# Performance work log

Measured on AMD Instinct MI355X. Metric: run time of the kernel, lower is better.

The kernel has to match this reference:

```python
import jax, jax.numpy as jnp
import numpy as np


def pairwise_distances(x):
    # x: [N, D] -> squared euclidean distances [N, N], clamped at 0
    sq = jnp.sum(x * x, axis=1)  # [N]
    dist = sq[:, None] + sq[None, :] - 2.0 * (x @ x.T)
    return jnp.maximum(dist, 0.0)


def setup_inputs() -> dict:
    key = jax.random.key(0)
    k1, k2 = jax.random.split(key)
    N, D, T = 8192, 128, 200000
    x = jax.random.normal(k1, (N, D), dtype=jnp.float32)
    triplets = jax.random.randint(k2, (T, 3), 0, N, dtype=jnp.int64)
    return {"x": x, "triplets": triplets}


def reference(x, triplets):
    dist = pairwise_distances(x)  # [N, N]
    i, j, k = triplets[:, 0], triplets[:, 1], triplets[:, 2]
    d_ij = dist[i, j]  # [T] anchor-positive distances
    d_ik = dist[i, k]  # [T] anchor-negative distances
    # loss = mean over triplets of log(1 + exp(d_ij - d_ik)) (uniform weights)
    loss = jnp.mean(jnp.log1p(jnp.exp(d_ij - d_ik)))
    return loss
```

## Files before the change

### kernel.cpp

```cpp
#include <hip/hip_runtime.h>
#include <math.h>

#define TRIP_BLOCKS 2048


template<int CTRL>
__device__ __forceinline__ float dpp_shr_add(float v) {
    int m = __builtin_amdgcn_update_dpp(0, __float_as_int(v), CTRL, 0xf, 0xf, true);
    return v + __int_as_float(m);
}

__device__ __forceinline__ float row16_sum(float v) {
    v = dpp_shr_add<0x111>(v);
    v = dpp_shr_add<0x112>(v);
    v = dpp_shr_add<0x114>(v);
    v = dpp_shr_add<0x118>(v);
    return v;
}

__device__ __forceinline__ float softplus_stable(float z) {
    return fmaxf(z, 0.0f) + log1pf(expf(-fabsf(z)));
}

__device__ __forceinline__ void sq_diff(const float4 a, const float4 b, float& acc) {
    float t;
    t = a.x - b.x; acc = fmaf(t, t, acc);
    t = a.y - b.y; acc = fmaf(t, t, acc);
    t = a.z - b.z; acc = fmaf(t, t, acc);
    t = a.w - b.w; acc = fmaf(t, t, acc);
}

__global__ void __launch_bounds__(256)
trip_kernel(const float* __restrict__ x, const int* __restrict__ trip,
            float* __restrict__ partial, int T) {
    const int lane    = threadIdx.x & 63;
    const int sub     = threadIdx.x & 15;
    const int gid     = (blockIdx.x * blockDim.x + threadIdx.x) >> 4;
    const int ngroups = (gridDim.x * blockDim.x) >> 4;

    const float4* xv = (const float4*)x;

    float local = 0.0f;
    for (int base = gid; base < T; base += 2 * ngroups) {
        int nA   = base;
        int nB   = base + ngroups;
        bool hasB = (nB < T);
        int nBc  = hasB ? nB : nA;

        int iA = trip[3 * nA], jA = trip[3 * nA + 1], kA = trip[3 * nA + 2];
        int iB = trip[3 * nBc], jB = trip[3 * nBc + 1], kB = trip[3 * nBc + 2];

        float4 aA0 = xv[iA * 32 + sub], aA1 = xv[iA * 32 + sub + 16];
        float4 bA0 = xv[jA * 32 + sub], bA1 = xv[jA * 32 + sub + 16];
        float4 cA0 = xv[kA * 32 + sub], cA1 = xv[kA * 32 + sub + 16];
        float4 aB0 = xv[iB * 32 + sub], aB1 = xv[iB * 32 + sub + 16];
        float4 bB0 = xv[jB * 32 + sub], bB1 = xv[jB * 32 + sub + 16];
        float4 cB0 = xv[kB * 32 + sub], cB1 = xv[kB * 32 + sub + 16];

        float d1A = 0.0f, d2A = 0.0f, d1B = 0.0f, d2B = 0.0f;
        sq_diff(aA0, bA0, d1A); sq_diff(aA1, bA1, d1A);
        sq_diff(aA0, cA0, d2A); sq_diff(aA1, cA1, d2A);
        sq_diff(aB0, bB0, d1B); sq_diff(aB1, bB1, d1B);
        sq_diff(aB0, cB0, d2B); sq_diff(aB1, cB1, d2B);

        d1A = row16_sum(d1A); d2A = row16_sum(d2A);
        d1B = row16_sum(d1B); d2B = row16_sum(d2B);

        if (sub == 15) {
            local += softplus_stable(d1A - d2A);
            if (hasB) local += softplus_stable(d1B - d2B);
        }
    }

    local += __shfl_xor(local, 16, 64);
    local += __shfl_xor(local, 32, 64);

    __shared__ float wsum[4];
    int wid = threadIdx.x >> 6;
    if (lane == 15) wsum[wid] = local;
    __syncthreads();
    if (threadIdx.x == 0)
        partial[blockIdx.x] = wsum[0] + wsum[1] + wsum[2] + wsum[3];
}

__global__ void __launch_bounds__(256)
finalize_kernel(const float* __restrict__ partial, int nparts,
                float* __restrict__ out, int T) {
    float s = 0.0f;
    for (int idx = threadIdx.x; idx < nparts; idx += 256)
        s += partial[idx];
#pragma unroll
    for (int off = 32; off; off >>= 1) s += __shfl_xor(s, off, 64);
    __shared__ float wsum[4];
    int wid = threadIdx.x >> 6;
    if ((threadIdx.x & 63) == 0) wsum[wid] = s;
    __syncthreads();
    if (threadIdx.x == 0)
        out[0] = (wsum[0] + wsum[1] + wsum[2] + wsum[3]) / (float)T;
}

extern "C" void kernel_launch(void* const* d_in, const int* in_sizes, int n_in,
                              void* d_out, int out_size, void* d_ws, size_t ws_size,
                              hipStream_t stream) {
    const float* x    = (const float*)d_in[0];
    const int*   trip = (const int*)d_in[1];
    float*       out  = (float*)d_out;

    int T = in_sizes[1] / 3;

    float* partial = (float*)d_ws;

    trip_kernel<<<TRIP_BLOCKS, 256, 0, stream>>>(x, trip, partial, T);
    finalize_kernel<<<1, 256, 0, stream>>>(partial, TRIP_BLOCKS, out, T);
}
```

Measured before the change: 78.20 us.

## Software-pipeline triplet index loads, drop dual-triplet unroll, use fast softplus

Replaces the two-triplets-per-iteration unroll with a single-triplet loop that prefetches the next triplet's indices while the current row gathers are in flight. The stable softplus switches to the fast __expf/__logf intrinsics, and the group count becomes a compile-time constant. The aim is to hide the dependent index-then-gather latency and cut transcendental cost. In exchange there are fewer independent gathers in flight per thread, slightly lower precision, and the code assumes the grid size always equals TRIP_BLOCKS.

```diff
diff --git a/kernel.cpp b/kernel.cpp
--- a/kernel.cpp
+++ b/kernel.cpp
@@ -18,8 +18,9 @@
     return v;
 }
 
-__device__ __forceinline__ float softplus_stable(float z) {
-    return fmaxf(z, 0.0f) + log1pf(expf(-fabsf(z)));
+__device__ __forceinline__ float softplus_fast(float z) {
+    float u = __expf(-fabsf(z));
+    return fmaxf(z, 0.0f) + __logf(1.0f + u);
 }
 
 __device__ __forceinline__ void sq_diff(const float4 a, const float4 b, float& acc) {
@@ -36,40 +37,41 @@
     const int lane    = threadIdx.x & 63;
     const int sub     = threadIdx.x & 15;
     const int gid     = (blockIdx.x * blockDim.x + threadIdx.x) >> 4;
-    const int ngroups = (gridDim.x * blockDim.x) >> 4;
+    const int ngroups = (TRIP_BLOCKS * 256) >> 4;
 
     const float4* xv = (const float4*)x;
 
     float local = 0.0f;
-    for (int base = gid; base < T; base += 2 * ngroups) {
-        int nA   = base;
-        int nB   = base + ngroups;
-        bool hasB = (nB < T);
-        int nBc  = hasB ? nB : nA;
 
-        int iA = trip[3 * nA], jA = trip[3 * nA + 1], kA = trip[3 * nA + 2];
-        int iB = trip[3 * nBc], jB = trip[3 * nBc + 1], kB = trip[3 * nBc + 2];
+    int n = gid;
+    int i = 0, j = 0, k = 0;
+    if (n < T) {
+        i = trip[3 * n];
+        j = trip[3 * n + 1];
+        k = trip[3 * n + 2];
+    }
+    while (n < T) {
+        float4 a0 = xv[i * 32 + sub], a1 = xv[i * 32 + sub + 16];
+        float4 b0 = xv[j * 32 + sub], b1 = xv[j * 32 + sub + 16];
+        float4 c0 = xv[k * 32 + sub], c1 = xv[k * 32 + sub + 16];
 
-        float4 aA0 = xv[iA * 32 + sub], aA1 = xv[iA * 32 + sub + 16];
-        float4 bA0 = xv[jA * 32 + sub], bA1 = xv[jA * 32 + sub + 16];
-        float4 cA0 = xv[kA * 32 + sub], cA1 = xv[kA * 32 + sub + 16];
-        float4 aB0 = xv[iB * 32 + sub], aB1 = xv[iB * 32 + sub + 16];
-        float4 bB0 = xv[jB * 32 + sub], bB1 = xv[jB * 32 + sub + 16];
-        float4 cB0 = xv[kB * 32 + sub], cB1 = xv[kB * 32 + sub + 16];
+        int n2 = n + ngroups;
+        if (n2 < T) {
+            i = trip[3 * n2];
+            j = trip[3 * n2 + 1];
+            k = trip[3 * n2 + 2];
+        }
 
-        float d1A = 0.0f, d2A = 0.0f, d1B = 0.0f, d2B = 0.0f;
-        sq_diff(aA0, bA0, d1A); sq_diff(aA1, bA1, d1A);
-        sq_diff(aA0, cA0, d2A); sq_diff(aA1, cA1, d2A);
-        sq_diff(aB0, bB0, d1B); sq_diff(aB1, bB1, d1B);
-        sq_diff(aB0, cB0, d2B); sq_diff(aB1, cB1, d2B);
+        float d1 = 0.0f, d2 = 0.0f;
+        sq_diff(a0, b0, d1); sq_diff(a1, b1, d1);
+        sq_diff(a0, c0, d2); sq_diff(a1, c1, d2);
 
-        d1A = row16_sum(d1A); d2A = row16_sum(d2A);
-        d1B = row16_sum(d1B); d2B = row16_sum(d2B);
+        d1 = row16_sum(d1);
+        d2 = row16_sum(d2);
+        if (sub == 15)
+            local += softplus_fast(d1 - d2);
 
-        if (sub == 15) {
-            local += softplus_stable(d1A - d2A);
-            if (hasB) local += softplus_stable(d1B - d2B);
-        }
+        n = n2;
     }
 
     local += __shfl_xor(local, 16, 64);
```

Result: faster. 74.54 us (-4.7%).

## Prefetch next triplet indices, fuse distance difference, use fast softplus

Applied to the files above, without the earlier changes.

Software-pipelines the triplet index loads by fetching the next iteration's indices before the current gathers are computed. It also folds d_ij - d_ik into one accumulator, which halves the DPP row reductions, and swaps log1pf/expf for the __expf/__logf intrinsics. The grid-size constant is hardcoded, so the kernel now depends on being launched with TRIP_BLOCKS blocks. The fast intrinsics trade some accuracy, and the fused accumulation changes the floating-point rounding order.

```diff
diff --git a/kernel.cpp b/kernel.cpp
--- a/kernel.cpp
+++ b/kernel.cpp
@@ -18,16 +18,9 @@
     return v;
 }
 
-__device__ __forceinline__ float softplus_stable(float z) {
-    return fmaxf(z, 0.0f) + log1pf(expf(-fabsf(z)));
-}
-
-__device__ __forceinline__ void sq_diff(const float4 a, const float4 b, float& acc) {
-    float t;
-    t = a.x - b.x; acc = fmaf(t, t, acc);
-    t = a.y - b.y; acc = fmaf(t, t, acc);
-    t = a.z - b.z; acc = fmaf(t, t, acc);
-    t = a.w - b.w; acc = fmaf(t, t, acc);
+__device__ __forceinline__ float softplus_fast(float z) {
+    float u = __expf(-fabsf(z));
+    return fmaxf(z, 0.0f) + __logf(1.0f + u);
 }
 
 __global__ void __launch_bounds__(256)
@@ -36,20 +29,21 @@
     const int lane    = threadIdx.x & 63;
     const int sub     = threadIdx.x & 15;
     const int gid     = (blockIdx.x * blockDim.x + threadIdx.x) >> 4;
-    const int ngroups = (gridDim.x * blockDim.x) >> 4;
+    const int ngroups = (TRIP_BLOCKS * 256) >> 4;
 
     const float4* xv = (const float4*)x;
 
     float local = 0.0f;
-    for (int base = gid; base < T; base += 2 * ngroups) {
-        int nA   = base;
-        int nB   = base + ngroups;
-        bool hasB = (nB < T);
-        int nBc  = hasB ? nB : nA;
 
-        int iA = trip[3 * nA], jA = trip[3 * nA + 1], kA = trip[3 * nA + 2];
-        int iB = trip[3 * nBc], jB = trip[3 * nBc + 1], kB = trip[3 * nBc + 2];
-
+    int nA = gid;
+    int nB = gid + ngroups;
+    int iA = 0, jA = 0, kA = 0, iB = 0, jB = 0, kB = 0;
+    if (nA < T) {
+        int nBc = nB < T ? nB : nA;
+        iA = trip[3 * nA];  jA = trip[3 * nA + 1];  kA = trip[3 * nA + 2];
+        iB = trip[3 * nBc]; jB = trip[3 * nBc + 1]; kB = trip[3 * nBc + 2];
+    }
+    while (nA < T) {
         float4 aA0 = xv[iA * 32 + sub], aA1 = xv[iA * 32 + sub + 16];
         float4 bA0 = xv[jA * 32 + sub], bA1 = xv[jA * 32 + sub + 16];
         float4 cA0 = xv[kA * 32 + sub], cA1 = xv[kA * 32 + sub + 16];
@@ -57,19 +51,44 @@
         float4 bB0 = xv[jB * 32 + sub], bB1 = xv[jB * 32 + sub + 16];
         float4 cB0 = xv[kB * 32 + sub], cB1 = xv[kB * 32 + sub + 16];
 
-        float d1A = 0.0f, d2A = 0.0f, d1B = 0.0f, d2B = 0.0f;
-        sq_diff(aA0, bA0, d1A); sq_diff(aA1, bA1, d1A);
-        sq_diff(aA0, cA0, d2A); sq_diff(aA1, cA1, d2A);
-        sq_diff(aB0, bB0, d1B); sq_diff(aB1, bB1, d1B);
-        sq_diff(aB0, cB0, d2B); sq_diff(aB1, cB1, d2B);
+        bool hasB = nB < T;
 
-        d1A = row16_sum(d1A); d2A = row16_sum(d2A);
-        d1B = row16_sum(d1B); d2B = row16_sum(d2B);
+        int nA2 = nA + 2 * ngroups;
+        int nB2 = nB + 2 * ngroups;
+        if (nA2 < T) {
+            int nB2c = nB2 < T ? nB2 : nA2;
+            iA = trip[3 * nA2];  jA = trip[3 * nA2 + 1];  kA = trip[3 * nA2 + 2];
+            iB = trip[3 * nB2c]; jB = trip[3 * nB2c + 1]; kB = trip[3 * nB2c + 2];
+        }
 
+        float t1, t2, eA, eB;
+        t1 = aA0.x - bA0.x; t2 = aA0.x - cA0.x; eA = t1 * t1;       eA = fmaf(-t2, t2, eA);
+        t1 = aA0.y - bA0.y; t2 = aA0.y - cA0.y; eA = fmaf(t1, t1, eA); eA = fmaf(-t2, t2, eA);
+        t1 = aA0.z - bA0.z; t2 = aA0.z - cA0.z; eA = fmaf(t1, t1, eA); eA = fmaf(-t2, t2, eA);
+        t1 = aA0.w - bA0.w; t2 = aA0.w - cA0.w; eA = fmaf(t1, t1, eA); eA = fmaf(-t2, t2, eA);
+        t1 = aA1.x - bA1.x; t2 = aA1.x - cA1.x; eA = fmaf(t1, t1, eA); eA = fmaf(-t2, t2, eA);
+        t1 = aA1.y - bA1.y; t2 = aA1.y - cA1.y; eA = fmaf(t1, t1, eA); eA = fmaf(-t2, t2, eA);
+        t1 = aA1.z - bA1.z; t2 = aA1.z - cA1.z; eA = fmaf(t1, t1, eA); eA = fmaf(-t2, t2, eA);
+        t1 = aA1.w - bA1.w; t2 = aA1.w - cA1.w; eA = fmaf(t1, t1, eA); eA = fmaf(-t2, t2, eA);
+
+        t1 = aB0.x - bB0.x; t2 = aB0.x - cB0.x; eB = t1 * t1;       eB = fmaf(-t2, t2, eB);
+        t1 = aB0.y - bB0.y; t2 = aB0.y - cB0.y; eB = fmaf(t1, t1, eB); eB = fmaf(-t2, t2, eB);
+        t1 = aB0.z - bB0.z; t2 = aB0.z - cB0.z; eB = fmaf(t1, t1, eB); eB = fmaf(-t2, t2, eB);
+        t1 = aB0.w - bB0.w; t2 = aB0.w - cB0.w; eB = fmaf(t1, t1, eB); eB = fmaf(-t2, t2, eB);
+        t1 = aB1.x - bB1.x; t2 = aB1.x - cB1.x; eB = fmaf(t1, t1, eB); eB = fmaf(-t2, t2, eB);
+        t1 = aB1.y - bB1.y; t2 = aB1.y - cB1.y; eB = fmaf(t1, t1, eB); eB = fmaf(-t2, t2, eB);
+        t1 = aB1.z - bB1.z; t2 = aB1.z - cB1.z; eB = fmaf(t1, t1, eB); eB = fmaf(-t2, t2, eB);
+        t1 = aB1.w - bB1.w; t2 = aB1.w - cB1.w; eB = fmaf(t1, t1, eB); eB = fmaf(-t2, t2, eB);
+
+        eA = row16_sum(eA);
+        eB = row16_sum(eB);
         if (sub == 15) {
-            local += softplus_stable(d1A - d2A);
-            if (hasB) local += softplus_stable(d1B - d2B);
+            local += softplus_fast(eA);
+            if (hasB) local += softplus_fast(eB);
         }
+
+        nA = nA2;
+        nB = nB2;
     }
 
     local += __shfl_xor(local, 16, 64);
```

New measurement: 75.39 us. 1.04x faster.
